# Optimization experiments

Measured on AMD Instinct MI355X. Metric: run time of the kernel, lower is better.

Reference implementation:

```python
import jax, jax.numpy as jnp
import numpy as np

B, T, H = 32, 4096, 512


def setup_inputs() -> dict:
    key = jax.random.key(0)
    k1, k2, k3, k4, k5 = jax.random.split(key, 5)
    stdv = 1.0 / np.sqrt(2 * H)
    stdv_v = 1.0 / np.sqrt(H)
    return {
        "hidden": jax.random.normal(k1, (B, H), dtype=jnp.float32),
        "encoder_outputs": jax.random.normal(k2, (T, B, H), dtype=jnp.float32),
        "W_attn": jax.random.uniform(k3, (H, 2 * H), minval=-stdv, maxval=stdv, dtype=jnp.float32),
        "b_attn": jax.random.uniform(k4, (H,), minval=-stdv, maxval=stdv, dtype=jnp.float32),
        "v": jax.random.uniform(k5, (H,), minval=-stdv_v, maxval=stdv_v, dtype=jnp.float32),
    }


def reference(hidden, encoder_outputs, W_attn, b_attn, v):
    # hidden: [B, H]; encoder_outputs: [T, B, H]
    T_ = encoder_outputs.shape[0]
    h = jnp.broadcast_to(hidden[None, :, :], (T_,) + hidden.shape).transpose(1, 0, 2)  # [B,T,H]
    enc = encoder_outputs.transpose(1, 0, 2)  # [B,T,H]
    cat = jnp.concatenate([h, enc], axis=2)  # [B,T,2H]
    # Linear(2H -> H) then legacy F.softmax with implicit dim=0 for 3D input (batch axis)
    energy = jax.nn.softmax(jnp.einsum('btk,hk->bth', cat, W_attn) + b_attn, axis=0)  # [B,T,H]
    # bmm(v[B,1,H], energy^T[B,H,T]) -> [B,1,T] -> squeeze -> [B,T]
    scores = jnp.einsum('h,bth->bt', v, energy)
    return jax.nn.relu(scores)[:, None, :]  # [B,1,T]
```

## Files before the change

kernel.cpp:

```cpp
#include <hip/hip_runtime.h>
#include <hip/hip_bf16.h>

#define B_ 32
#define T_ 4096
#define H_ 512
#define M_TILE 64
#define NTHREADS 512

typedef __attribute__((ext_vector_type(4))) short short4v;
typedef __attribute__((ext_vector_type(8))) short short8;
typedef __attribute__((ext_vector_type(8))) __bf16 bf16x8;
typedef __attribute__((ext_vector_type(4))) float f32x4;

__device__ __forceinline__ short f2bf(float f) {
    unsigned u = __builtin_bit_cast(unsigned, f);
    u = (u + 0x7fffu + ((u >> 16) & 1u)) >> 16;
    return (short)u;
}

__device__ __forceinline__ short4v pack4(f32x4 a) {
    union { unsigned u[2]; short4v s; } r;
    asm("v_cvt_pk_bf16_f32 %0, %1, %2" : "=v"(r.u[0]) : "v"(a[0]), "v"(a[1]));
    asm("v_cvt_pk_bf16_f32 %0, %1, %2" : "=v"(r.u[1]) : "v"(a[2]), "v"(a[3]));
    return r.s;
}

__global__ void prep_w2f(const float* __restrict__ W, short* __restrict__ w2f) {
    int idx = blockIdx.x * 256 + threadIdx.x;
    int j    = idx & 7;
    int lane = (idx >> 3) & 63;
    int ni   = (idx >> 9) & 3;
    int ck   = (idx >> 11) & 15;
    int c    = (idx >> 15) & 7;
    int h = c * 64 + ni * 16 + (lane & 15);
    int k = ck * 32 + (lane >> 4) * 8 + j;
    w2f[idx] = f2bf(W[h * (2 * H_) + H_ + k]);
}

__global__ void prep_hid(const float* __restrict__ hidden,
                         const float* __restrict__ W,
                         const float* __restrict__ bias,
                         float* __restrict__ hidproj) {
    __shared__ float hrow[H_];
    int b = blockIdx.y;
    int h = blockIdx.x * 128 + threadIdx.x;
    for (int i = threadIdx.x; i < H_; i += 128) hrow[i] = hidden[b * H_ + i];
    __syncthreads();
    const float* wr = W + (size_t)h * (2 * H_);
    float acc = bias[h];
#pragma unroll 4
    for (int k = 0; k < H_; k += 4) {
        acc += hrow[k]     * wr[k];
        acc += hrow[k + 1] * wr[k + 1];
        acc += hrow[k + 2] * wr[k + 2];
        acc += hrow[k + 3] * wr[k + 3];
    }
    hidproj[b * H_ + h] = acc;
}

__global__ __launch_bounds__(NTHREADS, 4)
void attn_main(const float* __restrict__ enc,
               const float* __restrict__ hidproj,
               const short* __restrict__ w2f,
               const float* __restrict__ vvec,
               float* __restrict__ out)
{
    __shared__ __align__(16) short lds_a[M_TILE * H_];

    const int tid  = threadIdx.x;
    const int lane = tid & 63;
    const int wid  = tid >> 6;
    const int lo   = lane & 15;
    const int hi4  = lane >> 4;
    const int t0   = blockIdx.x * 2;

    {
        const float* sp = enc + (size_t)blockIdx.x * (M_TILE * H_) + tid * 4;
        const int th    = tid >> 7;
        const int half  = (tid & 1) * 8;
        const int cb    = (tid & 127) >> 1;
        char* lb = (char*)lds_a;
#define ST(I, X) { short4v p = pack4(X); \
        *(short4v*)(lb + ((I)*4 + th) * 1024 + ((cb ^ (((I)*4 + th) & 7)) * 16) + half) = p; }
        f32x4 x0  = *(const f32x4*)(sp +  0 * 2048);
        f32x4 x1  = *(const f32x4*)(sp +  1 * 2048);
        f32x4 x2  = *(const f32x4*)(sp +  2 * 2048);
        f32x4 x3  = *(const f32x4*)(sp +  3 * 2048);
        f32x4 x4  = *(const f32x4*)(sp +  4 * 2048);
        f32x4 x5  = *(const f32x4*)(sp +  5 * 2048);
        f32x4 x6  = *(const f32x4*)(sp +  6 * 2048);
        f32x4 x7  = *(const f32x4*)(sp +  7 * 2048);
        ST(0, x0) ST(1, x1) ST(2, x2) ST(3, x3)
        f32x4 x8  = *(const f32x4*)(sp +  8 * 2048);
        f32x4 x9  = *(const f32x4*)(sp +  9 * 2048);
        f32x4 x10 = *(const f32x4*)(sp + 10 * 2048);
        f32x4 x11 = *(const f32x4*)(sp + 11 * 2048);
        ST(4, x4) ST(5, x5) ST(6, x6) ST(7, x7)
        f32x4 x12 = *(const f32x4*)(sp + 12 * 2048);
        f32x4 x13 = *(const f32x4*)(sp + 13 * 2048);
        f32x4 x14 = *(const f32x4*)(sp + 14 * 2048);
        f32x4 x15 = *(const f32x4*)(sp + 15 * 2048);
        ST(8, x8) ST(9, x9) ST(10, x10) ST(11, x11)
        ST(12, x12) ST(13, x13) ST(14, x14) ST(15, x15)
#undef ST
    }
    __syncthreads();

    f32x4 acc[4][4];
#pragma unroll
    for (int i = 0; i < 4; ++i)
#pragma unroll
        for (int j = 0; j < 4; ++j) acc[i][j] = f32x4{0.f, 0.f, 0.f, 0.f};

    const short* wbase = w2f + (size_t)wid * 32768 + lane * 8;
    const int xm = lo & 7;

#define KSUB(S4, BQ)                                                              \
    {                                                                             \
        bf16x8 af[4];                                                             \
        _Pragma("unroll")                                                         \
        for (int mi = 0; mi < 4; ++mi) {                                          \
            int r = mi * 16 + lo;                                                 \
            af[mi] = *(const bf16x8*)&lds_a[r * 512 + (((S4) + hi4) ^ xm) * 8];   \
        }                                                                         \
        __builtin_amdgcn_s_setprio(1);                                            \
        _Pragma("unroll")                                                         \
        for (int mi = 0; mi < 4; ++mi)                                            \
            _Pragma("unroll")                                                     \
            for (int ni = 0; ni < 4; ++ni)                                        \
                acc[mi][ni] = __builtin_amdgcn_mfma_f32_16x16x32_bf16(            \
                    af[mi], BQ[ni], acc[mi][ni], 0, 0, 0);                        \
        __builtin_amdgcn_s_setprio(0);                                            \
    }

    bf16x8 bqA[4], bqB[4];
#pragma unroll
    for (int ni = 0; ni < 4; ++ni) bqA[ni] = *(const bf16x8*)(wbase + (0 * 4 + ni) * 512);

#pragma unroll 1
    for (int kk = 0; kk < 8; ++kk) {
        const int s0 = kk * 2;
#pragma unroll
        for (int ni = 0; ni < 4; ++ni)
            bqB[ni] = *(const bf16x8*)(wbase + ((s0 + 1) * 4 + ni) * 512);
        KSUB(s0 * 4, bqA)
        if (kk < 7) {
#pragma unroll
            for (int ni = 0; ni < 4; ++ni)
                bqA[ni] = *(const bf16x8*)(wbase + ((s0 + 2) * 4 + ni) * 512);
        }
        KSUB((s0 + 1) * 4, bqB)
    }
#undef KSUB

    {
        float hp[2][4][4];
#pragma unroll
        for (int par = 0; par < 2; ++par)
#pragma unroll
            for (int j = 0; j < 4; ++j) {
                int b = par * 16 + hi4 * 4 + j;
#pragma unroll
                for (int ni = 0; ni < 4; ++ni)
                    hp[par][j][ni] = hidproj[b * H_ + wid * 64 + ni * 16 + lo];
            }
#pragma unroll
        for (int mi = 0; mi < 4; ++mi)
#pragma unroll
            for (int ni = 0; ni < 4; ++ni)
#pragma unroll
                for (int j = 0; j < 4; ++j)
                    acc[mi][ni][j] += hp[mi & 1][j][ni];
    }

    float vh[4];
#pragma unroll
    for (int ni = 0; ni < 4; ++ni) vh[ni] = vvec[wid * 64 + ni * 16 + lo];

    float scp[4][4];
#pragma unroll
    for (int tl2 = 0; tl2 < 2; ++tl2) {
        const int m0 = tl2 * 2, m1 = tl2 * 2 + 1;
#pragma unroll
        for (int ni = 0; ni < 4; ++ni) {
            float mx = -1e30f;
#pragma unroll
            for (int j = 0; j < 4; ++j) {
                mx = fmaxf(mx, acc[m0][ni][j]);
                mx = fmaxf(mx, acc[m1][ni][j]);
            }
            mx = fmaxf(mx, __shfl_xor(mx, 16));
            mx = fmaxf(mx, __shfl_xor(mx, 32));
            float e0[4], e1[4];
            float sum = 0.f;
#pragma unroll
            for (int j = 0; j < 4; ++j) {
                e0[j] = __expf(acc[m0][ni][j] - mx);
                e1[j] = __expf(acc[m1][ni][j] - mx);
                sum += e0[j] + e1[j];
            }
            sum += __shfl_xor(sum, 16);
            sum += __shfl_xor(sum, 32);
            float rs = vh[ni] / sum;
#pragma unroll
            for (int j = 0; j < 4; ++j) {
                if (ni == 0) { scp[m0][j] = e0[j] * rs; scp[m1][j] = e1[j] * rs; }
                else         { scp[m0][j] += e0[j] * rs; scp[m1][j] += e1[j] * rs; }
            }
        }
    }

#pragma unroll
    for (int mi = 0; mi < 4; ++mi)
#pragma unroll
        for (int j = 0; j < 4; ++j) {
            float x = scp[mi][j];
            x += __shfl_xor(x, 1);
            x += __shfl_xor(x, 2);
            x += __shfl_xor(x, 4);
            x += __shfl_xor(x, 8);
            scp[mi][j] = x;
        }

    __syncthreads();
    float* red = (float*)&lds_a[0];
    if (lo == 0) {
#pragma unroll
        for (int mi = 0; mi < 4; ++mi)
#pragma unroll
            for (int j = 0; j < 4; ++j)
                red[wid * 64 + mi * 16 + hi4 * 4 + j] = scp[mi][j];
    }
    __syncthreads();
    if (tid < M_TILE) {
        float s = 0.f;
#pragma unroll
        for (int w = 0; w < 8; ++w) s += red[w * 64 + tid];
        int b   = tid & 31;
        int tl2 = tid >> 5;
        out[(size_t)b * T_ + (t0 + tl2)] = fmaxf(s, 0.f);
    }
}

extern "C" void kernel_launch(void* const* d_in, const int* in_sizes, int n_in,
                              void* d_out, int out_size, void* d_ws, size_t ws_size,
                              hipStream_t stream) {
    const float* hidden = (const float*)d_in[0];
    const float* enc    = (const float*)d_in[1];
    const float* W      = (const float*)d_in[2];
    const float* bias   = (const float*)d_in[3];
    const float* v      = (const float*)d_in[4];
    float* out = (float*)d_out;

    float* hidproj = (float*)d_ws;
    short* w2f     = (short*)((char*)d_ws + 65536);

    prep_w2f<<<1024, 256, 0, stream>>>(W, w2f);
    prep_hid<<<dim3(4, 32), 128, 0, stream>>>(hidden, W, bias, hidproj);
    attn_main<<<T_ * B_ / (M_TILE), NTHREADS, 0, stream>>>(enc, hidproj, w2f, v, out);
}
```

Before: 116.0 us.

## Make attention kernel persistent with double-buffered LDS and prefetched encoder tiles

Replaces the one-tile-per-block launch (2048 blocks) with 256 persistent blocks that each process 8 consecutive tiles. Encoder tiles are double-buffered in LDS and the next tile's global loads are issued mid-GEMM, overlapping HBM traffic with MFMA work. Hidden projection and v are hoisted out of the tile loop, and the LDS write layout changes to 16-byte packed stores. The cost is one block per CU at 128KB+ LDS, so latency hiding depends entirely on intra-block overlap, and the 256 blocks must map evenly onto the CUs for good balance.

```diff
diff --git a/kernel.cpp b/kernel.cpp
--- a/kernel.cpp
+++ b/kernel.cpp
@@ -5,9 +5,10 @@
 #define T_ 4096
 #define H_ 512
 #define M_TILE 64
+#define TPB 8
+#define NBLK 256
 #define NTHREADS 512
 
-typedef __attribute__((ext_vector_type(4))) short short4v;
 typedef __attribute__((ext_vector_type(8))) short short8;
 typedef __attribute__((ext_vector_type(8))) __bf16 bf16x8;
 typedef __attribute__((ext_vector_type(4))) float f32x4;
@@ -18,10 +19,12 @@
     return (short)u;
 }
 
-__device__ __forceinline__ short4v pack4(f32x4 a) {
-    union { unsigned u[2]; short4v s; } r;
+__device__ __forceinline__ short8 pack8(f32x4 a, f32x4 b) {
+    union { unsigned u[4]; short8 s; } r;
     asm("v_cvt_pk_bf16_f32 %0, %1, %2" : "=v"(r.u[0]) : "v"(a[0]), "v"(a[1]));
     asm("v_cvt_pk_bf16_f32 %0, %1, %2" : "=v"(r.u[1]) : "v"(a[2]), "v"(a[3]));
+    asm("v_cvt_pk_bf16_f32 %0, %1, %2" : "=v"(r.u[2]) : "v"(b[0]), "v"(b[1]));
+    asm("v_cvt_pk_bf16_f32 %0, %1, %2" : "=v"(r.u[3]) : "v"(b[2]), "v"(b[3]));
     return r.s;
 }
 
@@ -58,62 +61,73 @@
     hidproj[b * H_ + h] = acc;
 }
 
-__global__ __launch_bounds__(NTHREADS, 4)
+__global__ __launch_bounds__(NTHREADS, 1)
 void attn_main(const float* __restrict__ enc,
                const float* __restrict__ hidproj,
                const short* __restrict__ w2f,
                const float* __restrict__ vvec,
                float* __restrict__ out)
 {
-    __shared__ __align__(16) short lds_a[M_TILE * H_];
+    __shared__ __align__(16) short lds_a[2][M_TILE * H_];
+    __shared__ float red[2][NTHREADS];
 
     const int tid  = threadIdx.x;
     const int lane = tid & 63;
     const int wid  = tid >> 6;
     const int lo   = lane & 15;
     const int hi4  = lane >> 4;
-    const int t0   = blockIdx.x * 2;
-
-    {
-        const float* sp = enc + (size_t)blockIdx.x * (M_TILE * H_) + tid * 4;
-        const int th    = tid >> 7;
-        const int half  = (tid & 1) * 8;
-        const int cb    = (tid & 127) >> 1;
-        char* lb = (char*)lds_a;
-#define ST(I, X) { short4v p = pack4(X); \
-        *(short4v*)(lb + ((I)*4 + th) * 1024 + ((cb ^ (((I)*4 + th) & 7)) * 16) + half) = p; }
-        f32x4 x0  = *(const f32x4*)(sp +  0 * 2048);
-        f32x4 x1  = *(const f32x4*)(sp +  1 * 2048);
-        f32x4 x2  = *(const f32x4*)(sp +  2 * 2048);
-        f32x4 x3  = *(const f32x4*)(sp +  3 * 2048);
-        f32x4 x4  = *(const f32x4*)(sp +  4 * 2048);
-        f32x4 x5  = *(const f32x4*)(sp +  5 * 2048);
-        f32x4 x6  = *(const f32x4*)(sp +  6 * 2048);
-        f32x4 x7  = *(const f32x4*)(sp +  7 * 2048);
-        ST(0, x0) ST(1, x1) ST(2, x2) ST(3, x3)
-        f32x4 x8  = *(const f32x4*)(sp +  8 * 2048);
-        f32x4 x9  = *(const f32x4*)(sp +  9 * 2048);
-        f32x4 x10 = *(const f32x4*)(sp + 10 * 2048);
-        f32x4 x11 = *(const f32x4*)(sp + 11 * 2048);
-        ST(4, x4) ST(5, x5) ST(6, x6) ST(7, x7)
-        f32x4 x12 = *(const f32x4*)(sp + 12 * 2048);
-        f32x4 x13 = *(const f32x4*)(sp + 13 * 2048);
-        f32x4 x14 = *(const f32x4*)(sp + 14 * 2048);
-        f32x4 x15 = *(const f32x4*)(sp + 15 * 2048);
-        ST(8, x8) ST(9, x9) ST(10, x10) ST(11, x11)
-        ST(12, x12) ST(13, x13) ST(14, x14) ST(15, x15)
-#undef ST
-    }
-    __syncthreads();
-
-    f32x4 acc[4][4];
-#pragma unroll
-    for (int i = 0; i < 4; ++i)
-#pragma unroll
-        for (int j = 0; j < 4; ++j) acc[i][j] = f32x4{0.f, 0.f, 0.f, 0.f};
+    const int xm   = lo & 7;
+    const int gbase = blockIdx.x * TPB;
+
+    const int aoff   = wid * 512 + lane * 8;
+    const int wr_off = (wid << 10) + ((lane ^ wid) << 4);
 
     const short* wbase = w2f + (size_t)wid * 32768 + lane * 8;
-    const int xm = lo & 7;
+
+    float hp[2][4][4];
+#pragma unroll
+    for (int par = 0; par < 2; ++par)
+#pragma unroll
+        for (int j = 0; j < 4; ++j) {
+            int b = par * 16 + hi4 * 4 + j;
+#pragma unroll
+            for (int ni = 0; ni < 4; ++ni)
+                hp[par][j][ni] = hidproj[b * H_ + wid * 64 + ni * 16 + lo];
+        }
+    float vh[4];
+#pragma unroll
+    for (int ni = 0; ni < 4; ++ni) vh[ni] = vvec[wid * 64 + ni * 16 + lo];
+
+    f32x4 sA0, sB0, sA1, sB1, sA2, sB2, sA3, sB3, sA4, sB4, sA5, sB5, sA6, sB6, sA7, sB7;
+
+#define LOADS(G)                                                                  \
+    { const float* ap_ = enc + (size_t)(G) * 32768 + aoff;                        \
+      sA0 = *(const f32x4*)(ap_ +     0); sB0 = *(const f32x4*)(ap_ +     4);     \
+      sA1 = *(const f32x4*)(ap_ +  4096); sB1 = *(const f32x4*)(ap_ +  4100);     \
+      sA2 = *(const f32x4*)(ap_ +  8192); sB2 = *(const f32x4*)(ap_ +  8196);     \
+      sA3 = *(const f32x4*)(ap_ + 12288); sB3 = *(const f32x4*)(ap_ + 12292);     \
+      sA4 = *(const f32x4*)(ap_ + 16384); sB4 = *(const f32x4*)(ap_ + 16388);     \
+      sA5 = *(const f32x4*)(ap_ + 20480); sB5 = *(const f32x4*)(ap_ + 20484);     \
+      sA6 = *(const f32x4*)(ap_ + 24576); sB6 = *(const f32x4*)(ap_ + 24580);     \
+      sA7 = *(const f32x4*)(ap_ + 28672); sB7 = *(const f32x4*)(ap_ + 28676); }
+
+#define WRITES(WB)                                                                \
+    { char* wbp_ = (char*)(WB) + wr_off;                                          \
+      *(short8*)(wbp_ +      0) = pack8(sA0, sB0);                                \
+      *(short8*)(wbp_ +   8192) = pack8(sA1, sB1);                                \
+      *(short8*)(wbp_ +  16384) = pack8(sA2, sB2);                                \
+      *(short8*)(wbp_ +  24576) = pack8(sA3, sB3);                                \
+      *(short8*)(wbp_ +  32768) = pack8(sA4, sB4);                                \
+      *(short8*)(wbp_ +  40960) = pack8(sA5, sB5);                                \
+      *(short8*)(wbp_ +  49152) = pack8(sA6, sB6);                                \
+      *(short8*)(wbp_ +  57344) = pack8(sA7, sB7); }
+
+    LOADS(gbase)
+    WRITES(&lds_a[0][0])
+    if (TPB > 1) LOADS(gbase + 1)
+    __builtin_amdgcn_sched_barrier(0);
+    asm volatile("s_waitcnt lgkmcnt(0)" ::: "memory");
+    __builtin_amdgcn_s_barrier();
 
 #define KSUB(S4, BQ)                                                              \
     {                                                                             \
@@ -121,7 +135,7 @@
         _Pragma("unroll")                                                         \
         for (int mi = 0; mi < 4; ++mi) {                                          \
             int r = mi * 16 + lo;                                                 \
-            af[mi] = *(const bf16x8*)&lds_a[r * 512 + (((S4) + hi4) ^ xm) * 8];   \
+            af[mi] = *(const bf16x8*)&rb[r * 512 + ((((S4) + hi4) ^ xm) << 3)];   \
         }                                                                         \
         __builtin_amdgcn_s_setprio(1);                                            \
         _Pragma("unroll")                                                         \
@@ -133,37 +147,48 @@
         __builtin_amdgcn_s_setprio(0);                                            \
     }
 
-    bf16x8 bqA[4], bqB[4];
-#pragma unroll
-    for (int ni = 0; ni < 4; ++ni) bqA[ni] = *(const bf16x8*)(wbase + (0 * 4 + ni) * 512);
+#define KSTEP(KK)                                                                 \
+    {                                                                             \
+        _Pragma("unroll")                                                         \
+        for (int ni = 0; ni < 4; ++ni)                                            \
+            bqB[ni] = *(const bf16x8*)(wbase + (((KK) * 2 + 1) * 4 + ni) * 512);  \
+        KSUB((KK) * 8, bqA)                                                       \
+        if ((KK) < 7) {                                                           \
+            _Pragma("unroll")                                                     \
+            for (int ni = 0; ni < 4; ++ni)                                        \
+                bqA[ni] = *(const bf16x8*)(wbase + (((KK) * 2 + 2) * 4 + ni) * 512); \
+        }                                                                         \
+        KSUB((KK) * 8 + 4, bqB)                                                   \
+    }
 
 #pragma unroll 1
-    for (int kk = 0; kk < 8; ++kk) {
-        const int s0 = kk * 2;
-#pragma unroll
-        for (int ni = 0; ni < 4; ++ni)
-            bqB[ni] = *(const bf16x8*)(wbase + ((s0 + 1) * 4 + ni) * 512);
-        KSUB(s0 * 4, bqA)
-        if (kk < 7) {
-#pragma unroll
-            for (int ni = 0; ni < 4; ++ni)
-                bqA[ni] = *(const bf16x8*)(wbase + ((s0 + 2) * 4 + ni) * 512);
-        }
-        KSUB((s0 + 1) * 4, bqB)
-    }
-#undef KSUB
-
-    {
-        float hp[2][4][4];
-#pragma unroll
-        for (int par = 0; par < 2; ++par)
-#pragma unroll
-            for (int j = 0; j < 4; ++j) {
-                int b = par * 16 + hi4 * 4 + j;
-#pragma unroll
-                for (int ni = 0; ni < 4; ++ni)
-                    hp[par][j][ni] = hidproj[b * H_ + wid * 64 + ni * 16 + lo];
+    for (int lt = 0; lt < TPB; ++lt) {
+        const int g = gbase + lt;
+        const short* __restrict__ rb = &lds_a[lt & 1][0];
+        short* __restrict__ wb = &lds_a[(lt & 1) ^ 1][0];
+
+        f32x4 acc[4][4];
+#pragma unroll
+        for (int i = 0; i < 4; ++i)
+#pragma unroll
+            for (int j = 0; j < 4; ++j) acc[i][j] = f32x4{0.f, 0.f, 0.f, 0.f};
+
+        bf16x8 bqA[4], bqB[4];
+#pragma unroll
+        for (int ni = 0; ni < 4; ++ni) bqA[ni] = *(const bf16x8*)(wbase + ni * 512);
+
+        KSTEP(0) KSTEP(1) KSTEP(2) KSTEP(3) KSTEP(4) KSTEP(5)
+
+        if (lt + 1 < TPB) {
+            WRITES(wb)
+            if (lt + 2 < TPB) {
+                LOADS(g + 2)
+                __builtin_amdgcn_sched_barrier(0);
             }
+        }
+
+        KSTEP(6) KSTEP(7)
+
 #pragma unroll
         for (int mi = 0; mi < 4; ++mi)
 #pragma unroll
@@ -171,75 +196,76 @@
 #pragma unroll
                 for (int j = 0; j < 4; ++j)
                     acc[mi][ni][j] += hp[mi & 1][j][ni];
-    }
-
-    float vh[4];
-#pragma unroll
-    for (int ni = 0; ni < 4; ++ni) vh[ni] = vvec[wid * 64 + ni * 16 + lo];
-
-    float scp[4][4];
-#pragma unroll
-    for (int tl2 = 0; tl2 < 2; ++tl2) {
-        const int m0 = tl2 * 2, m1 = tl2 * 2 + 1;
-#pragma unroll
-        for (int ni = 0; ni < 4; ++ni) {
-            float mx = -1e30f;
+
+        float scp[4][4];
+#pragma unroll
+        for (int tl2 = 0; tl2 < 2; ++tl2) {
+            const int m0 = tl2 * 2, m1 = tl2 * 2 + 1;
+#pragma unroll
+            for (int ni = 0; ni < 4; ++ni) {
+                float mx = -1e30f;
+#pragma unroll
+                for (int j = 0; j < 4; ++j) {
+                    mx = fmaxf(mx, acc[m0][ni][j]);
+                    mx = fmaxf(mx, acc[m1][ni][j]);
+                }
+                mx = fmaxf(mx, __shfl_xor(mx, 16));
+                mx = fmaxf(mx, __shfl_xor(mx, 32));
+                float e0[4], e1[4];
+                float sum = 0.f;
+#pragma unroll
+                for (int j = 0; j < 4; ++j) {
+                    e0[j] = __expf(acc[m0][ni][j] - mx);
+                    e1[j] = __expf(acc[m1][ni][j] - mx);
+                    sum += e0[j] + e1[j];
+                }
+                sum += __shfl_xor(sum, 16);
+                sum += __shfl_xor(sum, 32);
+                float rs = vh[ni] / sum;
+#pragma unroll
+                for (int j = 0; j < 4; ++j) {
+                    if (ni == 0) { scp[m0][j] = e0[j] * rs; scp[m1][j] = e1[j] * rs; }
+                    else         { scp[m0][j] += e0[j] * rs; scp[m1][j] += e1[j] * rs; }
+                }
+            }
+        }
+
+#pragma unroll
+        for (int mi = 0; mi < 4; ++mi)
 #pragma unroll
             for (int j = 0; j < 4; ++j) {
-                mx = fmaxf(mx, acc[m0][ni][j]);
-                mx = fmaxf(mx, acc[m1][ni][j]);
+                float x = scp[mi][j];
+                x += __shfl_xor(x, 1);
+                x += __shfl_xor(x, 2);
+                x += __shfl_xor(x, 4);
+                x += __shfl_xor(x, 8);
+                scp[mi][j] = x;
             }
-            mx = fmaxf(mx, __shfl_xor(mx, 16));
-            mx = fmaxf(mx, __shfl_xor(mx, 32));
-            float e0[4], e1[4];
-            float sum = 0.f;
-#pragma unroll
-            for (int j = 0; j < 4; ++j) {
-                e0[j] = __expf(acc[m0][ni][j] - mx);
-                e1[j] = __expf(acc[m1][ni][j] - mx);
-                sum += e0[j] + e1[j];
-            }
-            sum += __shfl_xor(sum, 16);
-            sum += __shfl_xor(sum, 32);
-            float rs = vh[ni] / sum;
-#pragma unroll
-            for (int j = 0; j < 4; ++j) {
-                if (ni == 0) { scp[m0][j] = e0[j] * rs; scp[m1][j] = e1[j] * rs; }
-                else         { scp[m0][j] += e0[j] * rs; scp[m1][j] += e1[j] * rs; }
-            }
-        }
-    }
-
-#pragma unroll
-    for (int mi = 0; mi < 4; ++mi)
-#pragma unroll
-        for (int j = 0; j < 4; ++j) {
-            float x = scp[mi][j];
-            x += __shfl_xor(x, 1);
-            x += __shfl_xor(x, 2);
-            x += __shfl_xor(x, 4);
-            x += __shfl_xor(x, 8);
-            scp[mi][j] = x;
-        }
-
-    __syncthreads();
-    float* red = (float*)&lds_a[0];
-    if (lo == 0) {
-#pragma unroll
-        for (int mi = 0; mi < 4; ++mi)
-#pragma unroll
-            for (int j = 0; j < 4; ++j)
-                red[wid * 64 + mi * 16 + hi4 * 4 + j] = scp[mi][j];
-    }
-    __syncthreads();
-    if (tid < M_TILE) {
-        float s = 0.f;
-#pragma unroll
-        for (int w = 0; w < 8; ++w) s += red[w * 64 + tid];
-        int b   = tid & 31;
-        int tl2 = tid >> 5;
-        out[(size_t)b * T_ + (t0 + tl2)] = fmaxf(s, 0.f);
-    }
+
+        if (lo == 0) {
+#pragma unroll
+            for (int mi = 0; mi < 4; ++mi)
+#pragma unroll
+                for (int j = 0; j < 4; ++j)
+                    red[lt & 1][wid * 64 + mi * 16 + hi4 * 4 + j] = scp[mi][j];
+        }
+
+        asm volatile("s_waitcnt lgkmcnt(0)" ::: "memory");
+        __builtin_amdgcn_s_barrier();
+
+        if (tid < M_TILE) {
+            float s = 0.f;
+#pragma unroll
+            for (int w = 0; w < 8; ++w) s += red[lt & 1][w * 64 + tid];
+            int b   = tid & 31;
+            int tl2 = tid >> 5;
+            out[(size_t)b * T_ + (g * 2 + tl2)] = fmaxf(s, 0.f);
+        }
+    }
+#undef KSTEP
+#undef KSUB
+#undef LOADS
+#undef WRITES
 }
 
 extern "C" void kernel_launch(void* const* d_in, const int* in_sizes, int n_in,
@@ -257,5 +283,5 @@
 
     prep_w2f<<<1024, 256, 0, stream>>>(W, w2f);
     prep_hid<<<dim3(4, 32), 128, 0, stream>>>(hidden, W, bias, hidproj);
-    attn_main<<<T_ * B_ / (M_TILE), NTHREADS, 0, stream>>>(enc, hidproj, w2f, v, out);
-}
+    attn_main<<<NBLK, NTHREADS, 0, stream>>>(enc, hidproj, w2f, v, out);
+}
```

After: 322.9 us. +178.2%, slower.
